# Optimization experiments

Measured on AMD Instinct MI355X. Metric: run time of the kernel, lower is better.

The kernel has to match this reference:

```python
import jax, jax.numpy as jnp
import numpy as np

D_NODE, D_EDGE, D_MODEL, TOPK, N_HEADS = 64, 16, 256, 5, 4
HEAD_DIM = D_MODEL // N_HEADS


def setup_inputs() -> dict:
    key = jax.random.key(0)
    ks = jax.random.split(key, 24)
    B, N = 256, 512
    E = N - 1
    def lin(k, fi, fo):
        k1, k2 = jax.random.split(k)
        s = 1.0 / np.sqrt(fi)
        return (jax.random.uniform(k1, (fi, fo), jnp.float32, -s, s),
                jax.random.uniform(k2, (fo,), jnp.float32, -s, s))
    Wn, bn = lin(ks[0], 8, D_NODE)
    We, be = lin(ks[1], 3, D_EDGE)
    Wq, bq = lin(ks[2], D_NODE, D_MODEL)
    Wkv, bkv = lin(ks[3], 2 * D_NODE + D_EDGE, 2 * D_MODEL)
    # MultiheadAttention in/out projections (fixed shared weights)
    Wiq, biq = lin(ks[4], D_MODEL, D_MODEL)
    Wik, bik = lin(ks[5], D_MODEL, D_MODEL)
    Wiv, biv = lin(ks[6], D_MODEL, D_MODEL)
    Wo, bo = lin(ks[7], D_MODEL, D_MODEL)
    Wf1, bf1 = lin(ks[8], D_NODE + D_MODEL, D_MODEL)
    Wf2, bf2 = lin(ks[9], D_MODEL, D_MODEL)
    Ws1, bs1 = lin(ks[10], D_NODE + D_EDGE + D_MODEL, D_MODEL)
    Ws2, bs2 = lin(ks[11], D_MODEL, 1 + 6 * D_MODEL)
    node_raw = jax.random.normal(ks[12], (B, N, 8), jnp.float32)
    edge_raw = jax.random.normal(ks[13], (B, E, 3), jnp.float32)
    return dict(node_raw=node_raw, edge_raw=edge_raw, ego_id=0,
                Wn=Wn, bn=bn, We=We, be=be, Wq=Wq, bq=bq, Wkv=Wkv, bkv=bkv,
                Wiq=Wiq, biq=biq, Wik=Wik, bik=bik, Wiv=Wiv, biv=biv,
                Wo=Wo, bo=bo, Wf1=Wf1, bf1=bf1, Wf2=Wf2, bf2=bf2,
                Ws1=Ws1, bs1=bs1, Ws2=Ws2, bs2=bs2)


def reference(node_raw, edge_raw, ego_id,
              Wn, bn, We, be, Wq, bq, Wkv, bkv,
              Wiq, biq, Wik, bik, Wiv, biv, Wo, bo,
              Wf1, bf1, Wf2, bf2, Ws1, bs1, Ws2, bs2):
    B, N, _ = node_raw.shape
    E = N - 1
    ego_id = int(ego_id)
    idx = np.arange(N)
    neighbor_idx = jnp.asarray(idx[idx != ego_id])  # (E,)

    node_feat = node_raw @ Wn + bn                   # (B, N, d_node)
    edge_feat = edge_raw @ We + be                   # (B, E, d_edge)
    ego_feat = node_feat[:, ego_id]                  # (B, d_node)
    neighbor_feat = node_feat[:, neighbor_idx]       # (B, E, d_node)

    ego_bcast = jnp.broadcast_to(ego_feat[:, None, :], (B, E, D_NODE))
    edge_input = jnp.concatenate([ego_bcast, edge_feat, neighbor_feat], -1)

    Q = ego_feat @ Wq + bq                           # (B, d_model)
    kv = edge_input @ Wkv + bkv                      # (B, E, 2*d_model)
    K, V = kv[..., :D_MODEL], kv[..., D_MODEL:]

    # MultiheadAttention: single query per batch, E keys/values
    q = (Q @ Wiq + biq).reshape(B, N_HEADS, HEAD_DIM)
    k = (K @ Wik + bik).reshape(B, E, N_HEADS, HEAD_DIM)
    v = (V @ Wiv + biv).reshape(B, E, N_HEADS, HEAD_DIM)
    scores = jnp.einsum('bhd,behd->bhe', q, k) / np.sqrt(HEAD_DIM)
    attn = jax.nn.softmax(scores, axis=-1)           # (B, H, E)
    ctx = jnp.einsum('bhe,behd->bhd', attn, v).reshape(B, D_MODEL)
    c_ego = ctx @ Wo + bo                            # (B, d_model)

    h = jnp.concatenate([ego_feat, c_ego], -1)
    h_ego_prime = jax.nn.relu(h @ Wf1 + bf1) @ Wf2 + bf2  # (B, d_model)

    c_bcast = jnp.broadcast_to(c_ego[:, None, :], (B, E, D_MODEL))
    edge_input2 = jnp.concatenate([neighbor_feat, edge_feat, c_bcast], -1)
    score_out = jax.nn.relu(edge_input2 @ Ws1 + bs1) @ Ws2 + bs2  # (B,E,1+6*dm)
    score = score_out[..., 0]                        # (B, E)
    h_enc = score_out[..., 1:].reshape(B, E, 6, D_MODEL)

    topk_val, topk_idx = jax.lax.top_k(score, TOPK)  # (B, topk)
    selected = jnp.take_along_axis(h_enc, topk_idx[:, :, None, None], axis=1)
    alpha = jax.nn.softmax(topk_val, axis=-1)[:, :, None, None]  # (B,topk,1,1)
    selected = selected * alpha
    return h_ego_prime, selected, topk_idx, alpha
```

## Files before the change

### kernel.cpp

```cpp
#include <hip/hip_runtime.h>
#include <hip/hip_bf16.h>
#include <math.h>

constexpr int B = 256, NN = 512, EE = 511;

constexpr size_t F_NF    = 0;
constexpr size_t F_EF    = F_NF   + (size_t)B*NN*64;
constexpr size_t F_WCK   = F_EF   + (size_t)B*EE*16;
constexpr size_t F_BCK   = F_WCK  + 144*256;
constexpr size_t F_WCV   = F_BCK  + 256;
constexpr size_t F_BCV   = F_WCV  + 144*256;
constexpr size_t F_WQ2   = F_BCV  + 256;
constexpr size_t F_BQ2   = F_WQ2  + 64*256;
constexpr size_t F_Q     = F_BQ2  + 256;
constexpr size_t F_AW    = F_Q    + (size_t)B*256;
constexpr size_t F_C0    = F_AW   + (size_t)B*4*80;
constexpr size_t F_SC    = F_C0   + (size_t)B*4;
constexpr size_t F_US    = F_SC   + (size_t)B*4*EE;
constexpr size_t F_CEGO  = F_US   + (size_t)B*4*80;
constexpr size_t F_CVEC  = F_CEGO + (size_t)B*256;
constexpr size_t F_SC2   = F_CVEC + (size_t)B*256;
constexpr size_t F_ALPHA = F_SC2  + (size_t)B*EE;
constexpr size_t F_TKI   = F_ALPHA+ (size_t)B*5;
constexpr size_t F_HS    = F_SC;

constexpr size_t O_HEGO  = 0;
constexpr size_t O_SEL   = 65536;
constexpr size_t O_TKI   = 2031616;
constexpr size_t O_ALPHA = 2032896;

__global__ void k_fuse(const float* Wkv, const float* bkv, const float* Wik, const float* bik,
                       const float* Wiv, const float* biv, const float* Wq,  const float* bq,
                       const float* Wiq, const float* biq, float* ws){
  int t = blockIdx.x*256 + threadIdx.x;
  if (t < 36864){
    int r = t >> 8, c = t & 255;
    float a = 0.f;
    for (int m=0;m<256;m++) a += Wkv[(size_t)r*512+m] * Wik[(size_t)m*256+c];
    ws[F_WCK + t] = a;
  } else if (t < 37120){
    int c = t - 36864;
    float a = bik[c];
    for (int m=0;m<256;m++) a += bkv[m] * Wik[(size_t)m*256+c];
    ws[F_BCK + c] = a;
  } else if (t < 73984){
    int i = t - 37120; int r = i >> 8, c = i & 255;
    float a = 0.f;
    for (int m=0;m<256;m++) a += Wkv[(size_t)r*512+256+m] * Wiv[(size_t)m*256+c];
    ws[F_WCV + i] = a;
  } else if (t < 74240){
    int c = t - 73984;
    float a = biv[c];
    for (int m=0;m<256;m++) a += bkv[256+m] * Wiv[(size_t)m*256+c];
    ws[F_BCV + c] = a;
  } else if (t < 90624){
    int i = t - 74240; int r = i >> 8, c = i & 255;
    float a = 0.f;
    for (int m=0;m<256;m++) a += Wq[(size_t)r*256+m] * Wiq[(size_t)m*256+c];
    ws[F_WQ2 + i] = a;
  } else if (t < 90880){
    int c = t - 90624;
    float a = biq[c];
    for (int m=0;m<256;m++) a += bq[m] * Wiq[(size_t)m*256+c];
    ws[F_BQ2 + c] = a;
  }
}

__global__ void k_nf(const float* node_raw, const float* Wn, const float* bn, float* ws){
  size_t t = (size_t)blockIdx.x*256 + threadIdx.x;
  int j = (int)(t & 63); size_t row = t >> 6;
  float a = bn[j];
  #pragma unroll
  for (int i=0;i<8;i++) a += node_raw[row*8+i] * Wn[(size_t)i*64+j];
  ws[F_NF + t] = a;
}

__global__ void k_ef(const float* edge_raw, const float* We, const float* be, float* ws){
  size_t t = (size_t)blockIdx.x*256 + threadIdx.x;
  int j = (int)(t & 15); size_t row = t >> 4;
  float a = be[j];
  #pragma unroll
  for (int i=0;i<3;i++) a += edge_raw[row*3+i] * We[(size_t)i*16+j];
  ws[F_EF + t] = a;
}

__global__ void k_q(const int* ego_p, float* ws){
  int b = blockIdx.x, c = threadIdx.x;
  int ego = *ego_p;
  const float* egf = ws + F_NF + ((size_t)b*NN + ego)*64;
  const float* Wq2 = ws + F_WQ2;
  float a = ws[F_BQ2 + c];
  for (int i=0;i<64;i++) a += egf[i]*Wq2[(size_t)i*256+c];
  ws[F_Q + (size_t)b*256 + c] = a;
}

__global__ void k_head(const int* ego_p, float* ws){
  int b = blockIdx.x >> 2, h = blockIdx.x & 3;
  int tid = threadIdx.x;
  __shared__ float qh[64];
  __shared__ float red[256];
  if (tid < 64) qh[tid] = ws[F_Q + (size_t)b*256 + h*64 + tid];
  __syncthreads();
  const float* Wck = ws + F_WCK;
  float p = 0.f;
  size_t awbase = F_AW + ((size_t)(b*4+h))*80;
  if (tid < 64){
    const float* wr = Wck + (size_t)(80+tid)*256 + h*64;
    float a=0.f; for(int d=0;d<64;d++) a += wr[d]*qh[d];
    ws[awbase + tid] = a;
  } else if (tid < 80){
    int i = tid-64;
    const float* wr = Wck + (size_t)(64+i)*256 + h*64;
    float a=0.f; for(int d=0;d<64;d++) a += wr[d]*qh[d];
    ws[awbase + 64 + i] = a;
  } else if (tid < 144){
    int j = tid-80;
    const float* wr = Wck + (size_t)j*256 + h*64;
    float a=0.f; for(int d=0;d<64;d++) a += wr[d]*qh[d];
    int ego = *ego_p;
    p = ws[F_NF + ((size_t)b*NN+ego)*64 + j] * a;
  } else if (tid < 208){
    int d = tid-144;
    p = ws[F_BCK + h*64 + d] * qh[d];
  }
  red[tid]=p; __syncthreads();
  for (int s=128;s>0;s>>=1){ if(tid<s) red[tid]+=red[tid+s]; __syncthreads(); }
  if (tid==0) ws[F_C0 + b*4 + h] = red[0];
}

__global__ void k_scores(const int* ego_p, float* ws){
  int b = blockIdx.x, tid = threadIdx.x;
  __shared__ float awz[4][80];
  __shared__ float c0s[4];
  for (int l=tid; l<320; l+=256) awz[l/80][l%80] = ws[F_AW + (size_t)b*320 + l];
  if (tid<4) c0s[tid] = ws[F_C0 + b*4 + tid];
  __syncthreads();
  int ego = *ego_p;
  for (int e=tid; e<EE; e+=256){
    int node = e < ego ? e : e+1;
    const float4* nr = (const float4*)(ws + F_NF + ((size_t)b*NN+node)*64);
    const float4* er = (const float4*)(ws + F_EF + ((size_t)b*EE+e)*16);
    float s[4] = {c0s[0],c0s[1],c0s[2],c0s[3]};
    #pragma unroll
    for (int i=0;i<16;i++){
      float4 x = nr[i];
      #pragma unroll
      for (int h=0;h<4;h++)
        s[h] += x.x*awz[h][i*4] + x.y*awz[h][i*4+1] + x.z*awz[h][i*4+2] + x.w*awz[h][i*4+3];
    }
    #pragma unroll
    for (int i=0;i<4;i++){
      float4 x = er[i];
      #pragma unroll
      for (int h=0;h<4;h++)
        s[h] += x.x*awz[h][64+i*4] + x.y*awz[h][64+i*4+1] + x.z*awz[h][64+i*4+2] + x.w*awz[h][64+i*4+3];
    }
    #pragma unroll
    for (int h=0;h<4;h++) ws[F_SC + ((size_t)(b*4+h))*EE + e] = s[h]*0.125f;
  }
}

__global__ void k_softmax(float* ws){
  int bh = blockIdx.x, tid = threadIdx.x;
  float* s = ws + F_SC + (size_t)bh*EE;
  __shared__ float red[256];
  float v0 = tid<EE ? s[tid] : -INFINITY;
  float v1 = tid+256<EE ? s[tid+256] : -INFINITY;
  red[tid] = fmaxf(v0,v1); __syncthreads();
  for (int st=128;st>0;st>>=1){ if(tid<st) red[tid]=fmaxf(red[tid],red[tid+st]); __syncthreads(); }
  float m = red[0]; __syncthreads();
  float e0 = tid<EE ? expf(v0-m) : 0.f;
  float e1 = tid+256<EE ? expf(v1-m) : 0.f;
  red[tid] = e0+e1; __syncthreads();
  for (int st=128;st>0;st>>=1){ if(tid<st) red[tid]+=red[tid+st]; __syncthreads(); }
  float inv = 1.f/red[0];
  if (tid<EE) s[tid] = e0*inv;
  if (tid+256<EE) s[tid+256] = e1*inv;
}

__global__ void k_usum(const int* ego_p, float* ws){
  int b = blockIdx.x>>2, h = blockIdx.x&3, d = threadIdx.x;
  if (d >= 80) return;
  const float* at = ws + F_SC + ((size_t)(b*4+h))*EE;
  int ego = *ego_p;
  float a = 0.f;
  if (d < 64){
    const float* base = ws + F_NF + (size_t)b*NN*64 + d;
    for (int e=0;e<EE;e++){
      int node = e<ego?e:e+1;
      a += at[e]*base[(size_t)node*64];
    }
  } else {
    const float* base = ws + F_EF + (size_t)b*EE*16 + (d-64);
    for (int e=0;e<EE;e++) a += at[e]*base[(size_t)e*16];
  }
  ws[F_US + ((size_t)(b*4+h))*80 + d] = a;
}

__global__ void k_bfinal(const int* ego_p,
                         const float* Wo, const float* bo,
                         const float* Wf1, const float* bf1p,
                         const float* Wf2, const float* bf2p,
                         const float* Ws1, const float* bs1,
                         float* ws, float* out){
  int b = blockIdx.x, t = threadIdx.x;
  __shared__ float ego_s[64], us_s[4][80], ctx_s[256], cego_s[256], hf_s[256];
  int ego = *ego_p;
  if (t < 64) ego_s[t] = ws[F_NF + ((size_t)b*NN+ego)*64 + t];
  for (int l=t; l<320; l+=256) us_s[l/80][l%80] = ws[F_US + (size_t)b*320 + l];
  __syncthreads();
  {
    int h = t >> 6;
    const float* Wcv = ws + F_WCV;
    float a = ws[F_BCV + t];
    for (int i=0;i<64;i++) a += ego_s[i]*Wcv[(size_t)i*256+t];
    for (int i=0;i<16;i++) a += us_s[h][64+i]*Wcv[(size_t)(64+i)*256+t];
    for (int i=0;i<64;i++) a += us_s[h][i]*Wcv[(size_t)(80+i)*256+t];
    ctx_s[t]=a;
  }
  __syncthreads();
  {
    float a = bo[t];
    for (int i=0;i<256;i++) a += ctx_s[i]*Wo[(size_t)i*256+t];
    cego_s[t]=a; ws[F_CEGO + (size_t)b*256+t]=a;
  }
  __syncthreads();
  {
    float a = bf1p[t];
    for (int i=0;i<64;i++)  a += ego_s[i]*Wf1[(size_t)i*256+t];
    for (int i=0;i<256;i++) a += cego_s[i]*Wf1[(size_t)(64+i)*256+t];
    hf_s[t]=fmaxf(a,0.f);
  }
  __syncthreads();
  {
    float a = bf2p[t];
    for (int i=0;i<256;i++) a += hf_s[i]*Wf2[(size_t)i*256+t];
    out[O_HEGO + (size_t)b*256+t] = a;
  }
  {
    float a = bs1[t];
    for (int i=0;i<256;i++) a += cego_s[i]*Ws1[(size_t)(80+i)*256+t];
    ws[F_CVEC + (size_t)b*256+t]=a;
  }
}

__global__ __launch_bounds__(512) void k_bigscore(const int* ego_p, const float* Ws1,
                                                  const float* Ws2, const float* bs2, float* ws){
  int tile = blockIdx.x, b = blockIdx.y;
  int tid = threadIdx.x;
  __shared__ float Fe[64][80];
  __shared__ float Bs[16][256];
  __shared__ float cv_s[256], w2_s[256];
  int ego = *ego_p;
  if (tid < 256){
    cv_s[tid] = ws[F_CVEC + (size_t)b*256 + tid];
    w2_s[tid] = Ws2[(size_t)tid*1537];
  }
  for (int l=tid; l<80*64; l+=512){
    int e = l/80, k = l - e*80;
    int eg = tile*64 + e;
    float v = 0.f;
    if (eg < EE){
      int node = eg<ego?eg:eg+1;
      v = (k<64) ? ws[F_NF + ((size_t)b*NN+node)*64 + k]
                 : ws[F_EF + ((size_t)b*EE+eg)*16 + (k-64)];
    }
    Fe[e][k] = v;
  }
  int tc = tid & 31, te = tid >> 5;
  float acc[4][8];
  #pragma unroll
  for (int i=0;i<4;i++)
    #pragma unroll
    for (int j=0;j<8;j++) acc[i][j]=0.f;

  for (int c=0;c<5;c++){
    __syncthreads();
    {
      float4* dst = (float4*)&Bs[0][0];
      const float4* s4 = (const float4*)(Ws1 + (size_t)(c*16)*256);
      dst[tid]       = s4[tid];
      dst[tid + 512] = s4[tid + 512];
    }
    __syncthreads();
    #pragma unroll
    for (int kk=0; kk<16; kk+=4){
      float A[4][4];
      #pragma unroll
      for (int i=0;i<4;i++){
        float4 t4 = *(const float4*)&Fe[te*4+i][c*16+kk];
        A[i][0]=t4.x; A[i][1]=t4.y; A[i][2]=t4.z; A[i][3]=t4.w;
      }
      #pragma unroll
      for (int q=0;q<4;q++){
        float4 b0 = *(const float4*)&Bs[kk+q][tc*8];
        float4 b1 = *(const float4*)&Bs[kk+q][tc*8+4];
        float bw[8] = {b0.x,b0.y,b0.z,b0.w,b1.x,b1.y,b1.z,b1.w};
        #pragma unroll
        for (int i=0;i<4;i++)
          #pragma unroll
          for (int j=0;j<8;j++) acc[i][j] = fmaf(A[i][q], bw[j], acc[i][j]);
      }
    }
  }
  float bs20 = bs2[0];
  #pragma unroll
  for (int i=0;i<4;i++){
    float p = 0.f;
    #pragma unroll
    for (int j=0;j<8;j++){
      float hcol = acc[i][j] + cv_s[tc*8+j];
      p += fmaxf(hcol,0.f)*w2_s[tc*8+j];
    }
    #pragma unroll
    for (int m=16;m>0;m>>=1) p += __shfl_xor(p, m, 64);
    if (tc==0){
      int eg = tile*64 + te*4 + i;
      if (eg < EE) ws[F_SC2 + (size_t)b*EE + eg] = p + bs20;
    }
  }
}

__global__ void k_topk(float* ws, float* out){
  int b = blockIdx.x, tid = threadIdx.x;
  __shared__ float sv[256]; __shared__ int si[256];
  __shared__ float tv[8];   __shared__ int tix[8];
  const float* s = ws + F_SC2 + (size_t)b*EE;
  float v0 = tid<EE ? s[tid] : -INFINITY;       int i0 = tid;
  float v1 = (tid+256)<EE ? s[tid+256] : -INFINITY; int i1 = tid+256;
  for (int t=0;t<5;t++){
    float bvv; int bii;
    if (v0 > v1 || (v0==v1 && i0<i1)){ bvv=v0; bii=i0; } else { bvv=v1; bii=i1; }
    sv[tid]=bvv; si[tid]=bii; __syncthreads();
    for (int st=128; st>0; st>>=1){
      if (tid<st){
        float ov=sv[tid+st]; int oi=si[tid+st];
        if (ov > sv[tid] || (ov==sv[tid] && oi<si[tid])){ sv[tid]=ov; si[tid]=oi; }
      }
      __syncthreads();
    }
    if (tid==0){ tv[t]=sv[0]; tix[t]=si[0]; }
    __syncthreads();
    int w = tix[t];
    if (i0==w) v0=-INFINITY;
    if (i1==w) v1=-INFINITY;
    __syncthreads();
  }
  if (tid==0){
    float m = tv[0];
    float ex[5]; float sum=0.f;
    for (int t=0;t<5;t++){ ex[t]=expf(tv[t]-m); sum+=ex[t]; }
    for (int t=0;t<5;t++){
      float al = ex[t]/sum;
      ws[F_ALPHA + (size_t)b*5+t] = al;
      ((int*)(ws + F_TKI))[b*5+t] = tix[t];
      out[O_TKI   + (size_t)b*5+t] = (float)tix[t];
      out[O_ALPHA + (size_t)b*5+t] = al;
    }
  }
}

__global__ void k_hid(const int* ego_p, const float* Ws1, float* ws){
  int bt = blockIdx.x;
  int b = bt/5;
  int tid = threadIdx.x;
  __shared__ float fr[80];
  int e = ((const int*)(ws+F_TKI))[bt];
  int ego = *ego_p;
  int node = e<ego ? e : e+1;
  if (tid < 64)      fr[tid] = ws[F_NF + ((size_t)b*NN+node)*64 + tid];
  else if (tid < 80) fr[tid] = ws[F_EF + ((size_t)b*EE+e)*16 + (tid-64)];
  __syncthreads();
  float a = ws[F_CVEC + (size_t)b*256 + tid];
  for (int d=0;d<80;d++) a += fr[d]*Ws1[(size_t)d*256+tid];
  ws[F_HS + (size_t)bt*256 + tid] = fmaxf(a,0.f);
}

__global__ __launch_bounds__(256) void k_enc(const float* Ws2, const float* bs2,
                                             float* ws, float* out){
  int r = blockIdx.x, g = blockIdx.y, tid = threadIdx.x;
  int n = r*256 + tid;
  __shared__ float hs[10][256];
  __shared__ float al[10];
  int b0 = g*2;
  for (int l=tid; l<10*256; l+=256)
    hs[l>>8][l&255] = ws[F_HS + ((size_t)b0*5)*256 + l];
  if (tid<10) al[tid] = ws[F_ALPHA + (size_t)b0*5 + tid];
  __syncthreads();
  float acc[10];
  #pragma unroll
  for (int i=0;i<10;i++) acc[i]=0.f;
  const float* w2p = Ws2 + 1 + n;
  for (int j=0;j<256;j+=4){
    float w0 = w2p[(size_t)(j+0)*1537];
    float w1 = w2p[(size_t)(j+1)*1537];
    float w2 = w2p[(size_t)(j+2)*1537];
    float w3 = w2p[(size_t)(j+3)*1537];
    #pragma unroll
    for (int i=0;i<10;i++){
      float4 h = *(const float4*)&hs[i][j];
      acc[i] = fmaf(h.x,w0, fmaf(h.y,w1, fmaf(h.z,w2, fmaf(h.w,w3, acc[i]))));
    }
  }
  float bb = bs2[1+n];
  #pragma unroll
  for (int i=0;i<10;i++)
    out[O_SEL + ((size_t)(b0*5+i))*1536 + n] = (acc[i]+bb)*al[i];
}

extern "C" void kernel_launch(void* const* d_in, const int* in_sizes, int n_in,
                              void* d_out, int out_size, void* d_ws, size_t ws_size,
                              hipStream_t stream){
  const float* node_raw=(const float*)d_in[0];
  const float* edge_raw=(const float*)d_in[1];
  const int*  ego_p   =(const int*)d_in[2];
  const float* Wn =(const float*)d_in[3];  const float* bn =(const float*)d_in[4];
  const float* We =(const float*)d_in[5];  const float* be =(const float*)d_in[6];
  const float* Wq =(const float*)d_in[7];  const float* bq =(const float*)d_in[8];
  const float* Wkv=(const float*)d_in[9];  const float* bkv=(const float*)d_in[10];
  const float* Wiq=(const float*)d_in[11]; const float* biq=(const float*)d_in[12];
  const float* Wik=(const float*)d_in[13]; const float* bik=(const float*)d_in[14];
  const float* Wiv=(const float*)d_in[15]; const float* biv=(const float*)d_in[16];
  const float* Wo =(const float*)d_in[17]; const float* bo =(const float*)d_in[18];
  const float* Wf1=(const float*)d_in[19]; const float* bf1p=(const float*)d_in[20];
  const float* Wf2=(const float*)d_in[21]; const float* bf2p=(const float*)d_in[22];
  const float* Ws1=(const float*)d_in[23]; const float* bs1=(const float*)d_in[24];
  const float* Ws2=(const float*)d_in[25]; const float* bs2=(const float*)d_in[26];
  float* ws=(float*)d_ws;
  float* out=(float*)d_out;

  k_fuse<<<355,256,0,stream>>>(Wkv,bkv,Wik,bik,Wiv,biv,Wq,bq,Wiq,biq,ws);
  k_nf<<<(B*NN*64)/256,256,0,stream>>>(node_raw,Wn,bn,ws);
  k_ef<<<(B*EE*16)/256,256,0,stream>>>(edge_raw,We,be,ws);
  k_q<<<B,256,0,stream>>>(ego_p,ws);
  k_head<<<B*4,256,0,stream>>>(ego_p,ws);
  k_scores<<<B,256,0,stream>>>(ego_p,ws);
  k_softmax<<<B*4,256,0,stream>>>(ws);
  k_usum<<<B*4,128,0,stream>>>(ego_p,ws);
  k_bfinal<<<B,256,0,stream>>>(ego_p,Wo,bo,Wf1,bf1p,Wf2,bf2p,Ws1,bs1,ws,out);
  k_bigscore<<<dim3(8,B),512,0,stream>>>(ego_p,Ws1,Ws2,bs2,ws);
  k_topk<<<B,256,0,stream>>>(ws,out);
  k_hid<<<B*5,256,0,stream>>>(ego_p,Ws1,ws);
  k_enc<<<dim3(6,128),256,0,stream>>>(Ws2,bs2,ws,out);
}
```

Before: 287.7 us.

## Fuse q projection into head, softmax with usum, split scores, fix Bs bank conflicts

Folds the per-batch q projection into k_head, so each head block computes its own 64 query columns and the separate k_q launch goes away. Merges the softmax and the weighted-sum (usum) kernels so the attention weights stay in shared memory instead of going back to global. Splits k_scores over two tiles per batch for more parallelism. Reindexes the Bs column reads in k_bigscore to tc*4 and 128+tc*4, aiming to reduce LDS bank conflicts. The cost is a few fewer launches and less global traffic, with slightly more redundant work per head block.

```diff
diff --git a/kernel.cpp b/kernel.cpp
--- a/kernel.cpp
+++ b/kernel.cpp
@@ -84,22 +84,19 @@
   ws[F_EF + t] = a;
 }
 
-__global__ void k_q(const int* ego_p, float* ws){
-  int b = blockIdx.x, c = threadIdx.x;
-  int ego = *ego_p;
-  const float* egf = ws + F_NF + ((size_t)b*NN + ego)*64;
-  const float* Wq2 = ws + F_WQ2;
-  float a = ws[F_BQ2 + c];
-  for (int i=0;i<64;i++) a += egf[i]*Wq2[(size_t)i*256+c];
-  ws[F_Q + (size_t)b*256 + c] = a;
-}
-
 __global__ void k_head(const int* ego_p, float* ws){
   int b = blockIdx.x >> 2, h = blockIdx.x & 3;
   int tid = threadIdx.x;
   __shared__ float qh[64];
   __shared__ float red[256];
-  if (tid < 64) qh[tid] = ws[F_Q + (size_t)b*256 + h*64 + tid];
+  int ego = *ego_p;
+  const float* egf = ws + F_NF + ((size_t)b*NN+ego)*64;
+  if (tid < 64){
+    int c = h*64 + tid;
+    float a = ws[F_BQ2 + c];
+    for (int i=0;i<64;i++) a += egf[i]*ws[F_WQ2 + (size_t)i*256 + c];
+    qh[tid] = a;
+  }
   __syncthreads();
   const float* Wck = ws + F_WCK;
   float p = 0.f;
@@ -117,8 +114,7 @@
     int j = tid-80;
     const float* wr = Wck + (size_t)j*256 + h*64;
     float a=0.f; for(int d=0;d<64;d++) a += wr[d]*qh[d];
-    int ego = *ego_p;
-    p = ws[F_NF + ((size_t)b*NN+ego)*64 + j] * a;
+    p = egf[j] * a;
   } else if (tid < 208){
     int d = tid-144;
     p = ws[F_BCK + h*64 + d] * qh[d];
@@ -129,72 +125,71 @@
 }
 
 __global__ void k_scores(const int* ego_p, float* ws){
-  int b = blockIdx.x, tid = threadIdx.x;
+  int tile = blockIdx.x, b = blockIdx.y, tid = threadIdx.x;
   __shared__ float awz[4][80];
   __shared__ float c0s[4];
   for (int l=tid; l<320; l+=256) awz[l/80][l%80] = ws[F_AW + (size_t)b*320 + l];
   if (tid<4) c0s[tid] = ws[F_C0 + b*4 + tid];
   __syncthreads();
-  int ego = *ego_p;
-  for (int e=tid; e<EE; e+=256){
-    int node = e < ego ? e : e+1;
-    const float4* nr = (const float4*)(ws + F_NF + ((size_t)b*NN+node)*64);
-    const float4* er = (const float4*)(ws + F_EF + ((size_t)b*EE+e)*16);
-    float s[4] = {c0s[0],c0s[1],c0s[2],c0s[3]};
-    #pragma unroll
-    for (int i=0;i<16;i++){
-      float4 x = nr[i];
-      #pragma unroll
-      for (int h=0;h<4;h++)
-        s[h] += x.x*awz[h][i*4] + x.y*awz[h][i*4+1] + x.z*awz[h][i*4+2] + x.w*awz[h][i*4+3];
-    }
-    #pragma unroll
-    for (int i=0;i<4;i++){
-      float4 x = er[i];
-      #pragma unroll
-      for (int h=0;h<4;h++)
-        s[h] += x.x*awz[h][64+i*4] + x.y*awz[h][64+i*4+1] + x.z*awz[h][64+i*4+2] + x.w*awz[h][64+i*4+3];
-    }
-    #pragma unroll
-    for (int h=0;h<4;h++) ws[F_SC + ((size_t)(b*4+h))*EE + e] = s[h]*0.125f;
-  }
-}
-
-__global__ void k_softmax(float* ws){
-  int bh = blockIdx.x, tid = threadIdx.x;
-  float* s = ws + F_SC + (size_t)bh*EE;
+  int e = tile*256 + tid;
+  if (e >= EE) return;
+  int ego = *ego_p;
+  int node = e < ego ? e : e+1;
+  const float4* nr = (const float4*)(ws + F_NF + ((size_t)b*NN+node)*64);
+  const float4* er = (const float4*)(ws + F_EF + ((size_t)b*EE+e)*16);
+  float s[4] = {c0s[0],c0s[1],c0s[2],c0s[3]};
+  #pragma unroll
+  for (int i=0;i<16;i++){
+    float4 x = nr[i];
+    #pragma unroll
+    for (int h=0;h<4;h++)
+      s[h] += x.x*awz[h][i*4] + x.y*awz[h][i*4+1] + x.z*awz[h][i*4+2] + x.w*awz[h][i*4+3];
+  }
+  #pragma unroll
+  for (int i=0;i<4;i++){
+    float4 x = er[i];
+    #pragma unroll
+    for (int h=0;h<4;h++)
+      s[h] += x.x*awz[h][64+i*4] + x.y*awz[h][64+i*4+1] + x.z*awz[h][64+i*4+2] + x.w*awz[h][64+i*4+3];
+  }
+  #pragma unroll
+  for (int h=0;h<4;h++) ws[F_SC + ((size_t)(b*4+h))*EE + e] = s[h]*0.125f;
+}
+
+__global__ void k_attn(const int* ego_p, float* ws){
+  int bh = blockIdx.x; int b = bh>>2; int tid = threadIdx.x;
+  __shared__ float sc[512];
   __shared__ float red[256];
+  const float* s = ws + F_SC + (size_t)bh*EE;
   float v0 = tid<EE ? s[tid] : -INFINITY;
-  float v1 = tid+256<EE ? s[tid+256] : -INFINITY;
+  float v1 = (tid+256)<EE ? s[tid+256] : -INFINITY;
   red[tid] = fmaxf(v0,v1); __syncthreads();
   for (int st=128;st>0;st>>=1){ if(tid<st) red[tid]=fmaxf(red[tid],red[tid+st]); __syncthreads(); }
   float m = red[0]; __syncthreads();
   float e0 = tid<EE ? expf(v0-m) : 0.f;
-  float e1 = tid+256<EE ? expf(v1-m) : 0.f;
+  float e1 = (tid+256)<EE ? expf(v1-m) : 0.f;
   red[tid] = e0+e1; __syncthreads();
   for (int st=128;st>0;st>>=1){ if(tid<st) red[tid]+=red[tid+st]; __syncthreads(); }
   float inv = 1.f/red[0];
-  if (tid<EE) s[tid] = e0*inv;
-  if (tid+256<EE) s[tid+256] = e1*inv;
-}
-
-__global__ void k_usum(const int* ego_p, float* ws){
-  int b = blockIdx.x>>2, h = blockIdx.x&3, d = threadIdx.x;
-  if (d >= 80) return;
-  const float* at = ws + F_SC + ((size_t)(b*4+h))*EE;
-  int ego = *ego_p;
-  float a = 0.f;
-  if (d < 64){
-    const float* base = ws + F_NF + (size_t)b*NN*64 + d;
+  sc[tid] = e0*inv;
+  sc[tid+256] = e1*inv;
+  __syncthreads();
+  int ego = *ego_p;
+  if (tid < 64){
+    const float* base = ws + F_NF + (size_t)b*NN*64 + tid;
+    float a = 0.f;
     for (int e=0;e<EE;e++){
       int node = e<ego?e:e+1;
-      a += at[e]*base[(size_t)node*64];
-    }
-  } else {
-    const float* base = ws + F_EF + (size_t)b*EE*16 + (d-64);
-    for (int e=0;e<EE;e++) a += at[e]*base[(size_t)e*16];
-  }
-  ws[F_US + ((size_t)(b*4+h))*80 + d] = a;
+      a += sc[e]*base[(size_t)node*64];
+    }
+    ws[F_US + (size_t)bh*80 + tid] = a;
+  } else if (tid < 80){
+    int d = tid-64;
+    const float* base = ws + F_EF + (size_t)b*EE*16 + d;
+    float a = 0.f;
+    for (int e=0;e<EE;e++) a += sc[e]*base[(size_t)e*16];
+    ws[F_US + (size_t)bh*80 + tid] = a;
+  }
 }
 
 __global__ void k_bfinal(const int* ego_p,
@@ -293,8 +288,8 @@
       }
       #pragma unroll
       for (int q=0;q<4;q++){
-        float4 b0 = *(const float4*)&Bs[kk+q][tc*8];
-        float4 b1 = *(const float4*)&Bs[kk+q][tc*8+4];
+        float4 b0 = *(const float4*)&Bs[kk+q][tc*4];
+        float4 b1 = *(const float4*)&Bs[kk+q][128 + tc*4];
         float bw[8] = {b0.x,b0.y,b0.z,b0.w,b1.x,b1.y,b1.z,b1.w};
         #pragma unroll
         for (int i=0;i<4;i++)
@@ -308,9 +303,16 @@
   for (int i=0;i<4;i++){
     float p = 0.f;
     #pragma unroll
-    for (int j=0;j<8;j++){
-      float hcol = acc[i][j] + cv_s[tc*8+j];
-      p += fmaxf(hcol,0.f)*w2_s[tc*8+j];
+    for (int j=0;j<4;j++){
+      int col = tc*4 + j;
+      float hcol = acc[i][j] + cv_s[col];
+      p += fmaxf(hcol,0.f)*w2_s[col];
+    }
+    #pragma unroll
+    for (int j=0;j<4;j++){
+      int col = 128 + tc*4 + j;
+      float hcol = acc[i][4+j] + cv_s[col];
+      p += fmaxf(hcol,0.f)*w2_s[col];
     }
     #pragma unroll
     for (int m=16;m>0;m>>=1) p += __shfl_xor(p, m, 64);
@@ -432,11 +434,9 @@
   k_fuse<<<355,256,0,stream>>>(Wkv,bkv,Wik,bik,Wiv,biv,Wq,bq,Wiq,biq,ws);
   k_nf<<<(B*NN*64)/256,256,0,stream>>>(node_raw,Wn,bn,ws);
   k_ef<<<(B*EE*16)/256,256,0,stream>>>(edge_raw,We,be,ws);
-  k_q<<<B,256,0,stream>>>(ego_p,ws);
   k_head<<<B*4,256,0,stream>>>(ego_p,ws);
-  k_scores<<<B,256,0,stream>>>(ego_p,ws);
-  k_softmax<<<B*4,256,0,stream>>>(ws);
-  k_usum<<<B*4,128,0,stream>>>(ego_p,ws);
+  k_scores<<<dim3(2,B),256,0,stream>>>(ego_p,ws);
+  k_attn<<<B*4,256,0,stream>>>(ego_p,ws);
   k_bfinal<<<B,256,0,stream>>>(ego_p,Wo,bo,Wf1,bf1p,Wf2,bf2p,Ws1,bs1,ws,out);
   k_bigscore<<<dim3(8,B),512,0,stream>>>(ego_p,Ws1,Ws2,bs2,ws);
   k_topk<<<B,256,0,stream>>>(ws,out);
```

Result: faster. 245.7 us (-14.6%).
